# Kernel tuning notes

Hardware: AMD Instinct MI355X
Metric: run time of the kernel (lower is better)

The kernel has to match this reference:

```python
import jax, jax.numpy as jnp
import numpy as np

REGION = 70  # region_width == region_height == receptive_field


def _localize(score_map, img_h, score_h):
    # stride=1, window=1x1 -> region_score is just the channel-mean at each pixel.
    B, _, Hs, Ws = score_map.shape
    m = score_map.mean(axis=1).reshape(B, -1)  # [B, Hs*Ws], row-major over (dim2, dim3)
    # loop order (i outer over dim2, j inner over dim3) + strict-inequality updates
    # == first-occurrence argmax/argmin in row-major order.
    imax = jnp.argmax(m, axis=1)
    vmax = jnp.max(m, axis=1)
    imin = jnp.argmin(m, axis=1)
    vmin = jnp.min(m, axis=1)
    rx = (imax // Ws).astype(jnp.float32)
    ry = (imax % Ws).astype(jnp.float32)
    fx = (imin // Ws).astype(jnp.float32)
    fy = (imin % Ws).astype(jnp.float32)
    # ax_tmp_real initialized to zeros (update iff score > 0); ax_tmp_fake to ones (iff score < 1)
    ax_real = jnp.where(vmax[:, None] > 0.0, jnp.stack([rx, ry], axis=1), 0.0)
    ax_fake = jnp.where(vmin[:, None] < 1.0, jnp.stack([fx, fy], axis=1), 1.0)
    img_stride = float((img_h - 70.0) // score_h)  # static python floor-div as in torch
    ax_real = ax_real * img_stride + 70.0
    ax_fake = ax_fake * img_stride + 70.0
    return ax_fake, ax_real


def _crop_one(img, row0, col0):
    # Faithful crop_and_resize (transform_fpcoor=True, crop size == box size == 70):
    # sample positions are row0 + [0..69], col0 + [0..69]; bilinear; zeros outside image.
    C, H, W = img.shape
    ys = row0 + jnp.arange(REGION, dtype=jnp.float32)
    xs = col0 + jnp.arange(REGION, dtype=jnp.float32)
    vy = (ys >= 0.0) & (ys <= H - 1.0)
    vx = (xs >= 0.0) & (xs <= W - 1.0)
    y0 = jnp.floor(ys)
    x0 = jnp.floor(xs)
    ly = ys - y0
    lx = xs - x0
    y0i = jnp.clip(y0.astype(jnp.int32), 0, H - 1)
    y1i = jnp.clip(y0i + 1, 0, H - 1)
    x0i = jnp.clip(x0.astype(jnp.int32), 0, W - 1)
    x1i = jnp.clip(x0i + 1, 0, W - 1)

    def gat(yi, xi):  # -> [C, 70, 70]
        return img[:, yi[:, None], xi[None, :]]

    top = gat(y0i, x0i) * (1.0 - lx)[None, None, :] + gat(y0i, x1i) * lx[None, None, :]
    bot = gat(y1i, x0i) * (1.0 - lx)[None, None, :] + gat(y1i, x1i) * lx[None, None, :]
    out = top * (1.0 - ly)[None, :, None] + bot * ly[None, :, None]
    mask = (vy[:, None] & vx[None, :]).astype(img.dtype)
    return out * mask[None]


_crop = jax.vmap(_crop_one)  # over batch


def _forward(real_B, fake_B, real_A, score_map):
    ax_fake, ax_real = _localize(score_map, real_B.shape[2], score_map.shape[2])
    ax_fake = jax.lax.stop_gradient(ax_fake)  # torch detaches via .cpu().numpy()
    ax_real = jax.lax.stop_gradient(ax_real)
    # boxes = [y, x, y+70, x+70] fed to RoIAlign as (x1,y1,x2,y2):
    # crop row start = ax[:,0] (the loop's _x, dim-2 index), col start = ax[:,1].
    fake_Bf = _crop(fake_B, ax_fake[:, 0], ax_fake[:, 1])
    real_Af = _crop(real_A, ax_fake[:, 0], ax_fake[:, 1])
    fake_ABf = jnp.concatenate((real_Af, fake_Bf), axis=1)
    fake_Br = _crop(fake_B, ax_real[:, 0], ax_real[:, 1])
    real_Ar = _crop(real_A, ax_real[:, 0], ax_real[:, 1])
    real_ABr = jnp.concatenate((real_Ar, fake_Br), axis=1)
    return (fake_Br, real_Ar, fake_Bf, real_Af, fake_ABf, real_ABr)


def setup_inputs() -> dict:
    key = jax.random.key(0)
    k1, k2, k3, k4 = jax.random.split(key, 4)
    B, H = 32, 512
    return {
        "real_B": jax.random.normal(k1, (B, 3, H, H), dtype=jnp.float32),
        "fake_B": jax.random.normal(k2, (B, 3, H, H), dtype=jnp.float32),
        "real_A": jax.random.normal(k3, (B, 3, H, H), dtype=jnp.float32),
        "score_map": jax.random.uniform(k4, (B, 1, 128, 128), dtype=jnp.float32),
    }


def reference(real_B, fake_B, real_A, score_map):
    return _forward(real_B, fake_B, real_A, score_map)
```

## Files before the change

### kernel.cpp

```cpp
#include <hip/hip_runtime.h>

#define SSZ   16384
#define SW    128
#define IMG   512
#define NPER  470400
#define OFF_AB_F 1881600
#define OFF_AB_R 2822400
#define NF4_BATCH 14700
#define CHUNKS 64
#define F4_PER_CHUNK 230

typedef float f4v __attribute__((ext_vector_type(4)));
typedef unsigned long long u64;

__device__ __forceinline__ unsigned ord_f32(float v) {
    unsigned s = __float_as_uint(v);
    return (s & 0x80000000u) ? ~s : (s | 0x80000000u);
}

__global__ __launch_bounds__(64)
void localize_partial(const float* __restrict__ score, u64* __restrict__ keys) {
    const int blk = blockIdx.x;
    const int b = blk >> 4, sl = blk & 15;
    const int t = threadIdx.x;
    const float4* p4 = (const float4*)(score + (size_t)b * SSZ + sl * 1024);

    float vmax = -__builtin_inff(); int imax = 0;
    float vmin =  __builtin_inff(); int imin = 0;
    #pragma unroll
    for (int q = 0; q < 4; ++q) {
        const float4 v = p4[t + 64 * q];
        const int e = sl * 1024 + (t + 64 * q) * 4;
        if (v.x > vmax) { vmax = v.x; imax = e;     }
        if (v.y > vmax) { vmax = v.y; imax = e + 1; }
        if (v.z > vmax) { vmax = v.z; imax = e + 2; }
        if (v.w > vmax) { vmax = v.w; imax = e + 3; }
        if (v.x < vmin) { vmin = v.x; imin = e;     }
        if (v.y < vmin) { vmin = v.y; imin = e + 1; }
        if (v.z < vmin) { vmin = v.z; imin = e + 2; }
        if (v.w < vmin) { vmin = v.w; imin = e + 3; }
    }
    #pragma unroll
    for (int off = 1; off < 64; off <<= 1) {
        const float mv = __shfl_xor(vmax, off); const int mi = __shfl_xor(imax, off);
        if (mv > vmax || (mv == vmax && mi < imax)) { vmax = mv; imax = mi; }
        const float nv = __shfl_xor(vmin, off); const int ni = __shfl_xor(imin, off);
        if (nv < vmin || (nv == vmin && ni < imin)) { vmin = nv; imin = ni; }
    }
    if (t == 0) {
        keys[b * 32 + sl]      = ((u64)ord_f32(vmax) << 32) | (unsigned)~imax;
        keys[b * 32 + 16 + sl] = ((u64)ord_f32(vmin) << 32) | (unsigned)imin;
    }
}

__global__ __launch_bounds__(256)
void crop_kernel(const float* __restrict__ fake_B,
                 const float* __restrict__ real_A,
                 const u64* __restrict__ keys,
                 float* __restrict__ out) {
    const int blk   = blockIdx.x;
    const int b     = blk / CHUNKS;
    const int chunk = blk % CHUNKS;
    const int t     = threadIdx.x;

    const u64* kb = keys + b * 32;
    u64 km = kb[0], kn = kb[16];
    #pragma unroll
    for (int s = 1; s < 16; ++s) {
        const u64 a = kb[s];      if (a > km) km = a;
        const u64 c = kb[16 + s]; if (c < kn) kn = c;
    }
    const unsigned uh = (unsigned)(km >> 32);
    const float bmax = __uint_as_float((uh & 0x80000000u) ? (uh & 0x7FFFFFFFu) : ~uh);
    const int bimax = (int)~(unsigned)km;
    const unsigned un = (unsigned)(kn >> 32);
    const float bmin = __uint_as_float((un & 0x80000000u) ? (un & 0x7FFFFFFFu) : ~un);
    const int bimin = (int)(unsigned)kn;

    int rr, rc, fr, fc;
    if (bmax > 0.0f) { rr = bimax / SW; rc = bimax % SW; } else { rr = 0; rc = 0; }
    if (bmin < 1.0f) { fr = bimin / SW; fc = bimin % SW; } else { fr = 1; fc = 1; }
    const int row0r = rr * 3 + 70, col0r = rc * 3 + 70;
    const int row0f = fr * 3 + 70, col0f = fc * 3 + 70;

    const size_t srcb = (size_t)b * 3 * (IMG * IMG);
    const int e0 = chunk * F4_PER_CHUNK;
    const int e1 = min(e0 + F4_PER_CHUNK, NF4_BATCH);
    for (int e = e0 + t; e < e1; e += 256) {
        const int k    = e / 3675;
        const int rem  = e - k * 3675;
        const int c    = rem / 1225;
        const int f4   = rem - c * 1225;
        const int flat = f4 * 4;
        const int i0   = flat / 70;
        const int j0   = flat - i0 * 70;

        const int row0 = (k < 2) ? row0r : row0f;
        const int col0 = (k < 2) ? col0r : col0f;
        const float* sp = ((k == 0 || k == 2) ? fake_B : real_A)
                          + srcb + (size_t)c * (IMG * IMG);
        f4v v;
        #pragma unroll
        for (int s = 0; s < 4; ++s) {
            int i = i0, j = j0 + s;
            if (j >= 70) { j -= 70; ++i; }
            const int y = row0 + i, x = col0 + j;
            v[s] = (y < IMG && x < IMG) ? sp[y * IMG + x] : 0.0f;
        }

        const size_t inner = (size_t)c * 4900 + flat;
        const size_t prim  = (size_t)k * NPER + (size_t)b * 14700 + inner;
        const size_t cb    = ((k < 2) ? (size_t)OFF_AB_R : (size_t)OFF_AB_F)
                             + (size_t)b * 29400
                             + ((k & 1) ? 0 : 3) * 4900
                             + inner;
        __builtin_nontemporal_store(v, (f4v*)(out + prim));
        __builtin_nontemporal_store(v, (f4v*)(out + cb));
    }
}

extern "C" void kernel_launch(void* const* d_in, const int* in_sizes, int n_in,
                              void* d_out, int out_size, void* d_ws, size_t ws_size,
                              hipStream_t stream) {
    const float* fake_B    = (const float*)d_in[1];
    const float* real_A    = (const float*)d_in[2];
    const float* score_map = (const float*)d_in[3];
    float* out = (float*)d_out;
    u64*   keys = (u64*)d_ws;

    localize_partial<<<32 * 16, 64, 0, stream>>>(score_map, keys);
    crop_kernel<<<32 * CHUNKS, 256, 0, stream>>>(fake_B, real_A, keys, out);
}
```

Measured before the change: 15.93 us.

## Fuse localize and crop into one cooperative kernel with grid sync

```diff
diff --git a/kernel.cpp b/kernel.cpp
--- a/kernel.cpp
+++ b/kernel.cpp
@@ -1,4 +1,7 @@
 #include <hip/hip_runtime.h>
+#include <hip/hip_cooperative_groups.h>
+
+namespace cg = cooperative_groups;
 
 #define SSZ   16384
 #define SW    128
@@ -7,8 +10,8 @@
 #define OFF_AB_F 1881600
 #define OFF_AB_R 2822400
 #define NF4_BATCH 14700
-#define CHUNKS 64
-#define F4_PER_CHUNK 230
+#define CHUNKS 16
+#define F4_PER_CHUNK 919
 
 typedef float f4v __attribute__((ext_vector_type(4)));
 typedef unsigned long long u64;
@@ -18,50 +21,59 @@
     return (s & 0x80000000u) ? ~s : (s | 0x80000000u);
 }
 
-__global__ __launch_bounds__(64)
-void localize_partial(const float* __restrict__ score, u64* __restrict__ keys) {
+__global__ __launch_bounds__(256)
+void fused_coop(const float* __restrict__ fake_B,
+                const float* __restrict__ real_A,
+                const float* __restrict__ score,
+                u64* __restrict__ keys,
+                float* __restrict__ out) {
     const int blk = blockIdx.x;
-    const int b = blk >> 4, sl = blk & 15;
-    const int t = threadIdx.x;
-    const float4* p4 = (const float4*)(score + (size_t)b * SSZ + sl * 1024);
+    const int b   = blk >> 4;
+    const int sl  = blk & 15;
+    const int t   = threadIdx.x;
 
-    float vmax = -__builtin_inff(); int imax = 0;
-    float vmin =  __builtin_inff(); int imin = 0;
-    #pragma unroll
-    for (int q = 0; q < 4; ++q) {
-        const float4 v = p4[t + 64 * q];
-        const int e = sl * 1024 + (t + 64 * q) * 4;
-        if (v.x > vmax) { vmax = v.x; imax = e;     }
+    __shared__ float sv[8];
+    __shared__ int   si[8];
+
+    {
+        const float4* p4 = (const float4*)(score + (size_t)b * SSZ + (size_t)sl * 1024);
+        const float4 v = p4[t];
+        const int e = sl * 1024 + t * 4;
+        float vmax = v.x; int imax = e;
+        float vmin = v.x; int imin = e;
         if (v.y > vmax) { vmax = v.y; imax = e + 1; }
         if (v.z > vmax) { vmax = v.z; imax = e + 2; }
         if (v.w > vmax) { vmax = v.w; imax = e + 3; }
-        if (v.x < vmin) { vmin = v.x; imin = e;     }
         if (v.y < vmin) { vmin = v.y; imin = e + 1; }
         if (v.z < vmin) { vmin = v.z; imin = e + 2; }
         if (v.w < vmin) { vmin = v.w; imin = e + 3; }
+        #pragma unroll
+        for (int off = 1; off < 64; off <<= 1) {
+            const float mv = __shfl_xor(vmax, off); const int mi = __shfl_xor(imax, off);
+            if (mv > vmax || (mv == vmax && mi < imax)) { vmax = mv; imax = mi; }
+            const float nv = __shfl_xor(vmin, off); const int ni = __shfl_xor(imin, off);
+            if (nv < vmin || (nv == vmin && ni < imin)) { vmin = nv; imin = ni; }
+        }
+        if ((t & 63) == 0) {
+            const int w = t >> 6;
+            sv[w]     = vmax; si[w]     = imax;
+            sv[w + 4] = vmin; si[w + 4] = imin;
+        }
+        __syncthreads();
+        if (t == 0) {
+            float bm = sv[0]; int bi = si[0];
+            float nm = sv[4]; int ni = si[4];
+            #pragma unroll
+            for (int w = 1; w < 4; ++w) {
+                if (sv[w] > bm || (sv[w] == bm && si[w] < bi)) { bm = sv[w]; bi = si[w]; }
+                if (sv[w+4] < nm || (sv[w+4] == nm && si[w+4] < ni)) { nm = sv[w+4]; ni = si[w+4]; }
+            }
+            keys[b * 32 + sl]      = ((u64)ord_f32(bm) << 32) | (unsigned)~bi;
+            keys[b * 32 + 16 + sl] = ((u64)ord_f32(nm) << 32) | (unsigned)ni;
+        }
     }
-    #pragma unroll
-    for (int off = 1; off < 64; off <<= 1) {
-        const float mv = __shfl_xor(vmax, off); const int mi = __shfl_xor(imax, off);
-        if (mv > vmax || (mv == vmax && mi < imax)) { vmax = mv; imax = mi; }
-        const float nv = __shfl_xor(vmin, off); const int ni = __shfl_xor(imin, off);
-        if (nv < vmin || (nv == vmin && ni < imin)) { vmin = nv; imin = ni; }
-    }
-    if (t == 0) {
-        keys[b * 32 + sl]      = ((u64)ord_f32(vmax) << 32) | (unsigned)~imax;
-        keys[b * 32 + 16 + sl] = ((u64)ord_f32(vmin) << 32) | (unsigned)imin;
-    }
-}
 
-__global__ __launch_bounds__(256)
-void crop_kernel(const float* __restrict__ fake_B,
-                 const float* __restrict__ real_A,
-                 const u64* __restrict__ keys,
-                 float* __restrict__ out) {
-    const int blk   = blockIdx.x;
-    const int b     = blk / CHUNKS;
-    const int chunk = blk % CHUNKS;
-    const int t     = threadIdx.x;
+    cg::this_grid().sync();
 
     const u64* kb = keys + b * 32;
     u64 km = kb[0], kn = kb[16];
@@ -84,7 +96,7 @@
     const int row0f = fr * 3 + 70, col0f = fc * 3 + 70;
 
     const size_t srcb = (size_t)b * 3 * (IMG * IMG);
-    const int e0 = chunk * F4_PER_CHUNK;
+    const int e0 = sl * F4_PER_CHUNK;
     const int e1 = min(e0 + F4_PER_CHUNK, NF4_BATCH);
     for (int e = e0 + t; e < e1; e += 256) {
         const int k    = e / 3675;
@@ -125,9 +137,11 @@
     const float* fake_B    = (const float*)d_in[1];
     const float* real_A    = (const float*)d_in[2];
     const float* score_map = (const float*)d_in[3];
-    float* out = (float*)d_out;
+    float* out  = (float*)d_out;
     u64*   keys = (u64*)d_ws;
 
-    localize_partial<<<32 * 16, 64, 0, stream>>>(score_map, keys);
-    crop_kernel<<<32 * CHUNKS, 256, 0, stream>>>(fake_B, real_A, keys, out);
+    void* args[] = { (void*)&fake_B, (void*)&real_A, (void*)&score_map,
+                     (void*)&keys, (void*)&out };
+    hipLaunchCooperativeKernel((void*)fused_coop, dim3(32 * CHUNKS), dim3(256),
+                               args, 0, stream);
 }
```

Result: slower. 61.82 us (+288.1%).
